# Kernel tuning notes

Hardware: AMD Instinct MI355X
Metric: run time of the kernel (lower is better)

Reference implementation:

```python
import jax, jax.numpy as jnp
import numpy as np
import math

D_FEAT = 256
D_EMB = 128
NUM_HEADS = 4
D_K = D_EMB // NUM_HEADS
N = 1024
SEQ = D_FEAT + 1


def _ln(x, g=None, b=None, eps=1e-5):
    m = jnp.mean(x, axis=-1, keepdims=True)
    v = jnp.mean((x - m) ** 2, axis=-1, keepdims=True)
    y = (x - m) / jnp.sqrt(v + eps)
    if g is None:
        return y
    return y * g + b


def setup_inputs() -> dict:
    key = jax.random.key(0)
    ks = jax.random.split(key, 16)
    s = 0.05  # init scale for linear weights
    inp = {
        "Z": jax.random.normal(ks[0], (N, D_FEAT), jnp.float32),
        "A_no_diag": jax.random.normal(ks[1], (SEQ, SEQ), jnp.float32),
        "feat_emb": jax.random.normal(ks[2], (D_FEAT, D_EMB), jnp.float32),
        "label_token": jax.random.normal(ks[3], (1, 1, D_EMB), jnp.float32),
        "Wq": jax.random.normal(ks[4], (D_EMB, D_EMB), jnp.float32) * s,
        "bq": jnp.zeros((D_EMB,), jnp.float32),
        "Wk": jax.random.normal(ks[5], (D_EMB, D_EMB), jnp.float32) * s,
        "bk": jnp.zeros((D_EMB,), jnp.float32),
        "Wv": jax.random.normal(ks[6], (D_EMB, D_EMB), jnp.float32) * s,
        "bv": jnp.zeros((D_EMB,), jnp.float32),
        "Wo": jax.random.normal(ks[7], (D_EMB, D_EMB), jnp.float32) * s,
        "bo": jnp.zeros((D_EMB,), jnp.float32),
        "W1": jax.random.normal(ks[8], (D_EMB, 2 * D_EMB), jnp.float32) * s,
        "b1": jnp.zeros((2 * D_EMB,), jnp.float32),
        "W2": jax.random.normal(ks[9], (2 * D_EMB, D_EMB), jnp.float32) * s,
        "b2": jnp.zeros((D_EMB,), jnp.float32),
        "g1": jnp.ones((D_EMB,), jnp.float32),
        "beta1": jnp.zeros((D_EMB,), jnp.float32),
        "g2": jnp.ones((D_EMB,), jnp.float32),
        "beta2": jnp.zeros((D_EMB,), jnp.float32),
        "alpha_res": jnp.asarray(0.5, jnp.float32),
    }
    return inp


def reference(Z, A_no_diag, feat_emb, label_token, Wq, bq, Wk, bk, Wv, bv,
              Wo, bo, W1, b1, W2, b2, g1, beta1, g2, beta2, alpha_res):
    n = Z.shape[0]
    # normalize raw features (no affine) over d_feat
    Z_norm = _ln(Z)                                   # [N, F]
    # outer-product feature embedding
    X_feats = Z_norm[:, :, None] * feat_emb[None]     # [N, F, E]
    label = jnp.broadcast_to(label_token, (n, 1, D_EMB))
    X = jnp.concatenate([X_feats, label], axis=1)     # [N, S, E]
    X_norm = _ln(X, g1, beta1)
    # QKV projections, split into heads
    Q = (X_norm @ Wq + bq).reshape(n, SEQ, NUM_HEADS, D_K)
    K = (X_norm @ Wk + bk).reshape(n, SEQ, NUM_HEADS, D_K)
    V = (X_norm @ Wv + bv).reshape(n, SEQ, NUM_HEADS, D_K)
    scores = jnp.einsum('nqhd,nkhd->nhqk', Q, K) / math.sqrt(D_K)
    # DAG additive log-mask
    cm = jnp.abs(A_no_diag).T
    c_max = jnp.max(cm)
    cm = jnp.where(c_max > 1e-6, cm / c_max, cm + 1e-3)
    di = jnp.arange(SEQ)
    cm = cm.at[di, di].set(1.0)
    dag_mask = jnp.log(cm + 1e-9)                     # [S, S]
    scores = scores + dag_mask[None, None]
    attn = jax.nn.softmax(scores, axis=-1)
    out = jnp.einsum('nhqk,nkhd->nqhd', attn, V).reshape(n, SEQ, D_EMB)
    out = out @ Wo + bo
    # FFN (dropout inactive in eval), exact GELU as torch default
    h = _ln(out, g2, beta2)
    ffn = jax.nn.gelu(h @ W1 + b1, approximate=False) @ W2 + b2
    Hn = out + ffn
    Z_final = alpha_res * Hn + X_norm
    return Z_final[:, -1, :]                          # [N, E]
```

## Files before the change

kernel.cpp:

```cpp
#include <hip/hip_runtime.h>
#include <hip/hip_bf16.h>
#include <math.h>

#define NSAMP 1024
#define F 256
#define E 128
#define SEQ 257
#define NH 4
#define DK 32

#define OFF_MASK   0
#define OFF_PMAX   264
#define OFF_A      512
#define OFF_B      1536
#define OFF_SCLAST 1540
#define OFF_CV     1544
#define OFF_VLAST  1672
#define OFF_XL     1800
#define OFF_VF     1928
#define OFF_MF     2184
#define OFF_UV     2560
#define OFF_SQ     35328
#define OFF_SK     35456
#define OFF_SCK    35584

__device__ inline float wave_sum(float v) {
#pragma unroll
    for (int off = 32; off >= 1; off >>= 1) v += __shfl_xor(v, off, 64);
    return v;
}
__device__ inline float wave_max(float v) {
#pragma unroll
    for (int off = 32; off >= 1; off >>= 1) v = fmaxf(v, __shfl_xor(v, off, 64));
    return v;
}
__device__ inline float gelu_exact(float x) {
    return 0.5f * x * (1.0f + erff(x * 0.7071067811865476f));
}

__global__ __launch_bounds__(128) void pre1_kernel(
    const float* __restrict__ A, const float* __restrict__ feat,
    const float* __restrict__ lab, const float* __restrict__ Wq,
    const float* __restrict__ bq, const float* __restrict__ Wk,
    const float* __restrict__ bk, const float* __restrict__ Wv,
    const float* __restrict__ bv, const float* __restrict__ g1,
    const float* __restrict__ beta1, float* __restrict__ ws)
{
    const int bid = blockIdx.x, tid = threadIdx.x;
    __shared__ float red[128];
    __shared__ float sv[128];

    if (bid < 128) {
        float m = 0.f;
        for (int i = bid * 128 + tid; i < SEQ * SEQ; i += 128 * 128)
            m = fmaxf(m, fabsf(A[i]));
        red[tid] = m;
        __syncthreads();
        for (int s = 64; s >= 1; s >>= 1) {
            if (tid < s) red[tid] = fmaxf(red[tid], red[tid + s]);
            __syncthreads();
        }
        if (tid == 0) ws[OFF_PMAX + bid] = red[0];
    } else if (bid < 384) {
        const int k = bid - 128;
        float f = feat[k * E + tid];
        red[tid] = f;
        __syncthreads();
        for (int s = 64; s >= 1; s >>= 1) { if (tid < s) red[tid] += red[tid + s]; __syncthreads(); }
        float mf = red[0] * (1.f / E);
        __syncthreads();
        float d = f - mf;
        red[tid] = d * d;
        __syncthreads();
        for (int s = 64; s >= 1; s >>= 1) { if (tid < s) red[tid] += red[tid + s]; __syncthreads(); }
        if (tid == 0) { ws[OFF_MF + k] = mf; ws[OFF_VF + k] = red[0] * (1.f / E); }
    } else {
        const int j = bid - 384;
        if (j < 3) {
            float lv = lab[tid];
            red[tid] = lv;
            __syncthreads();
            for (int s = 64; s >= 1; s >>= 1) { if (tid < s) red[tid] += red[tid + s]; __syncthreads(); }
            float lm = red[0] * (1.f / E);
            __syncthreads();
            float d = lv - lm;
            red[tid] = d * d;
            __syncthreads();
            for (int s = 64; s >= 1; s >>= 1) { if (tid < s) red[tid] += red[tid + s]; __syncthreads(); }
            float rstd = rsqrtf(red[0] * (1.f / E) + 1e-5f);
            __syncthreads();
            float x = d * rstd * g1[tid] + beta1[tid];
            sv[tid] = x;
            if (j == 0) ws[OFF_XL + tid] = x;
        } else {
            sv[tid] = beta1[tid];
        }
        __syncthreads();
        const float* W    = (j == 0) ? Wq : (j == 2 || j == 4) ? Wv : Wk;
        const float* bias = (j == 0) ? bq : (j == 2 || j == 4) ? bv : bk;
        float acc = 0.f;
#pragma unroll 8
        for (int e = 0; e < E; ++e) acc += sv[e] * W[e * E + tid];
        acc += bias[tid];
        const int off = (j == 0) ? OFF_SQ : (j == 1) ? OFF_SK : (j == 2) ? OFF_VLAST
                      : (j == 3) ? OFF_SCK : OFF_CV;
        ws[off + tid] = acc;
    }
}

__global__ __launch_bounds__(256) void pre23_kernel(
    const float* __restrict__ A, const float* __restrict__ feat,
    const float* __restrict__ g1, const float* __restrict__ Wk,
    const float* __restrict__ Wv, float* __restrict__ ws)
{
    const int bid = blockIdx.x, tid = threadIdx.x;
    __shared__ float su[128];
    __shared__ float sUK[128];
    __shared__ float red[256];

    if (bid < 256) {
        const int k = bid;
        if (tid < 128) {
            const float mf = ws[OFF_MF + k];
            su[tid] = (feat[k * E + tid] - mf) * g1[tid];
        }
        __syncthreads();
        {
            const int d = tid & 127;
            const float* W = (tid < 128) ? Wv : Wk;
            float acc = 0.f;
#pragma unroll 8
            for (int e = 0; e < E; ++e) acc += su[e] * W[e * E + d];
            if (tid < 128) ws[OFF_UV + k * E + d] = acc;
            else sUK[d] = acc;
        }
        __syncthreads();
        if (tid < 128) {
            float v = sUK[tid] * ws[OFF_SQ + tid];
#pragma unroll
            for (int off = 16; off >= 1; off >>= 1) v += __shfl_xor(v, off, 64);
            if ((tid & 31) == 0)
                ws[OFF_A + k * 4 + (tid >> 5)] = v * 0.17677669529663687f;
        }
    } else {
        float m = (tid < 128) ? ws[OFF_PMAX + tid] : 0.f;
        red[tid] = m;
        __syncthreads();
        for (int s = 128; s >= 1; s >>= 1) {
            if (tid < s) red[tid] = fmaxf(red[tid], red[tid + s]);
            __syncthreads();
        }
        const float cmax = red[0];
        {
            float v = fabsf(A[tid * SEQ + (SEQ - 1)]);
            float cmv = (cmax > 1e-6f) ? v / cmax : v + 1e-3f;
            ws[OFF_MASK + tid] = logf(cmv + 1e-9f);
        }
        if (tid < 128) su[tid]  = ws[OFF_SQ + tid];
        else           sUK[tid - 128] = ws[OFF_SK + tid - 128];
        if (tid < 128) red[tid] = ws[OFF_SCK + tid];
        __syncthreads();
        if (tid < NH) {
            const int h = tid;
            float bb = 0.f, sl = 0.f;
#pragma unroll
            for (int d = h * DK; d < (h + 1) * DK; ++d) {
                bb += su[d] * red[d];
                sl += su[d] * sUK[d];
            }
            const float rs = 0.17677669529663687f;
            ws[OFF_B + h] = bb * rs;
            ws[OFF_SCLAST + h] = sl * rs + logf(1.0f + 1e-9f);
        }
    }
}

__global__ __launch_bounds__(1024) void main_kernel(
    const float* __restrict__ Z, const float* __restrict__ Wo,
    const float* __restrict__ bo, const float* __restrict__ W1,
    const float* __restrict__ b1, const float* __restrict__ W2,
    const float* __restrict__ b2, const float* __restrict__ g2,
    const float* __restrict__ beta2, const float* __restrict__ alpha_p,
    const float* __restrict__ ws, float* __restrict__ out)
{
    const int tid = threadIdx.x;
    const int wv = tid >> 6, lane = tid & 63;
    const int n0 = blockIdx.x * 4;

    __shared__ float wm4[4][256][4];
    __shared__ float att4[128][4];
    __shared__ float oar[4][128];
    __shared__ float h24[128][4];
    __shared__ float gg4[256][4];
    __shared__ float red[4096];
    __shared__ float sSumP[4][4], sP256[4][4], sInv[4][4];

    if (wv < 4) {
        const int n = n0 + wv;
        float z[4];
#pragma unroll
        for (int i = 0; i < 4; ++i) z[i] = Z[n * F + lane + 64 * i];
        float sum = wave_sum(z[0] + z[1] + z[2] + z[3]);
        float mean = sum * (1.f / F);
        float ss = 0.f;
#pragma unroll
        for (int i = 0; i < 4; ++i) { float d = z[i] - mean; ss += d * d; }
        ss = wave_sum(ss);
        float rstd = rsqrtf(ss * (1.f / F) + 1e-5f);

        float tk[4], mk[4], areg[4][4];
#pragma unroll
        for (int i = 0; i < 4; ++i) {
            int k = lane + 64 * i;
            float s = (z[i] - mean) * rstd;
            float vf = ws[OFF_VF + k];
            tk[i] = s * rsqrtf(s * s * vf + 1e-5f);
            mk[i] = ws[OFF_MASK + k];
            float4 a4 = *(const float4*)(ws + OFF_A + k * 4);
            areg[i][0] = a4.x; areg[i][1] = a4.y; areg[i][2] = a4.z; areg[i][3] = a4.w;
        }
#pragma unroll
        for (int h = 0; h < 4; ++h) {
            float bh = ws[OFF_B + h];
            float scL = ws[OFF_SCLAST + h];
            float sc[4];
            float mx = -1e30f;
#pragma unroll
            for (int i = 0; i < 4; ++i) {
                sc[i] = tk[i] * areg[i][h] + bh + mk[i];
                mx = fmaxf(mx, sc[i]);
            }
            if (lane == 0) mx = fmaxf(mx, scL);
            mx = wave_max(mx);
            float local = 0.f;
            float p[4];
#pragma unroll
            for (int i = 0; i < 4; ++i) { p[i] = expf(sc[i] - mx); local += p[i]; }
            float sumP = wave_sum(local);
#pragma unroll
            for (int i = 0; i < 4; ++i) wm4[h][lane + 64 * i][wv] = p[i] * tk[i];
            if (lane == 0) {
                float p256 = expf(scL - mx);
                sSumP[wv][h] = sumP;
                sP256[wv][h] = p256;
                sInv[wv][h] = 1.f / (sumP + p256);
            }
        }
    }
    __syncthreads();

    const int g = tid >> 7;
    const int d = tid & 127;

    {
        const int h = d >> 5;
        float a0 = 0.f, a1 = 0.f, a2 = 0.f, a3 = 0.f;
        const float* uvp = ws + OFF_UV + (g * 32) * E + d;
#pragma unroll 8
        for (int kk = 0; kk < 32; ++kk) {
            float uv = uvp[kk * E];
            float4 w = *(const float4*)&wm4[h][g * 32 + kk][0];
            a0 += w.x * uv; a1 += w.y * uv; a2 += w.z * uv; a3 += w.w * uv;
        }
        float* r = red + g * 512 + d;
        r[0] = a0; r[128] = a1; r[256] = a2; r[384] = a3;
    }
    __syncthreads();
    if (tid < 512) {
        const int s = tid >> 7, dd = tid & 127, hh = dd >> 5;
        float v = 0.f;
#pragma unroll
        for (int gi = 0; gi < 8; ++gi) v += red[gi * 512 + s * 128 + dd];
        float cv = ws[OFF_CV + dd], vl = ws[OFF_VLAST + dd];
        att4[dd][s] = (v + sSumP[s][hh] * cv + sP256[s][hh] * vl) * sInv[s][hh];
    }
    __syncthreads();

    {
        float a0 = 0.f, a1 = 0.f, a2 = 0.f, a3 = 0.f;
        const float* wop = Wo + (g * 16) * E + d;
#pragma unroll 8
        for (int i = 0; i < 16; ++i) {
            float w = wop[i * E];
            float4 av = *(const float4*)&att4[g * 16 + i][0];
            a0 += av.x * w; a1 += av.y * w; a2 += av.z * w; a3 += av.w * w;
        }
        float* r = red + g * 512 + d;
        r[0] = a0; r[128] = a1; r[256] = a2; r[384] = a3;
    }
    __syncthreads();
    if (tid < 512) {
        const int s = tid >> 7, dd = tid & 127;
        float v = 0.f;
#pragma unroll
        for (int gi = 0; gi < 8; ++gi) v += red[gi * 512 + s * 128 + dd];
        oar[s][dd] = v + bo[dd];
    }
    __syncthreads();

    if (wv < 4) {
        float x0 = oar[wv][lane], x1 = oar[wv][lane + 64];
        float sum = wave_sum(x0 + x1);
        float mean = sum * (1.f / E);
        float d0 = x0 - mean, d1 = x1 - mean;
        float ss = wave_sum(d0 * d0 + d1 * d1);
        float rstd = rsqrtf(ss * (1.f / E) + 1e-5f);
        h24[lane][wv]      = d0 * rstd * g2[lane] + beta2[lane];
        h24[lane + 64][wv] = d1 * rstd * g2[lane + 64] + beta2[lane + 64];
    }
    __syncthreads();

    {
        const int grp = tid >> 8;
        const int j = tid & 255;
        float a0 = 0.f, a1 = 0.f, a2 = 0.f, a3 = 0.f;
        const float* w1p = W1 + (grp * 32) * (2 * E) + j;
#pragma unroll 8
        for (int i = 0; i < 32; ++i) {
            float w = w1p[i * (2 * E)];
            float4 hv = *(const float4*)&h24[grp * 32 + i][0];
            a0 += hv.x * w; a1 += hv.y * w; a2 += hv.z * w; a3 += hv.w * w;
        }
        float* r = red + grp * 1024 + j;
        r[0] = a0; r[256] = a1; r[512] = a2; r[768] = a3;
    }
    __syncthreads();
    {
        const int s = tid >> 8, j = tid & 255;
        float v = red[s * 256 + j] + red[1024 + s * 256 + j]
                + red[2048 + s * 256 + j] + red[3072 + s * 256 + j] + b1[j];
        gg4[j][s] = gelu_exact(v);
    }
    __syncthreads();

    {
        float a0 = 0.f, a1 = 0.f, a2 = 0.f, a3 = 0.f;
        const float* w2p = W2 + (g * 32) * E + d;
#pragma unroll 8
        for (int i = 0; i < 32; ++i) {
            float w = w2p[i * E];
            float4 gv = *(const float4*)&gg4[g * 32 + i][0];
            a0 += gv.x * w; a1 += gv.y * w; a2 += gv.z * w; a3 += gv.w * w;
        }
        float* r = red + g * 512 + d;
        r[0] = a0; r[128] = a1; r[256] = a2; r[384] = a3;
    }
    __syncthreads();
    if (tid < 512) {
        const int s = tid >> 7, dd = tid & 127;
        float f2 = b2[dd];
#pragma unroll
        for (int gi = 0; gi < 8; ++gi) f2 += red[gi * 512 + s * 128 + dd];
        float xl = ws[OFF_XL + dd];
        float alpha = alpha_p[0];
        out[(n0 + s) * E + dd] = alpha * (oar[s][dd] + f2) + xl;
    }
}

extern "C" void kernel_launch(void* const* d_in, const int* in_sizes, int n_in,
                              void* d_out, int out_size, void* d_ws, size_t ws_size,
                              hipStream_t stream) {
    const float* Z     = (const float*)d_in[0];
    const float* A     = (const float*)d_in[1];
    const float* feat  = (const float*)d_in[2];
    const float* lab   = (const float*)d_in[3];
    const float* Wq    = (const float*)d_in[4];
    const float* bq    = (const float*)d_in[5];
    const float* Wk    = (const float*)d_in[6];
    const float* bk    = (const float*)d_in[7];
    const float* Wv    = (const float*)d_in[8];
    const float* bv    = (const float*)d_in[9];
    const float* Wo    = (const float*)d_in[10];
    const float* bo    = (const float*)d_in[11];
    const float* W1    = (const float*)d_in[12];
    const float* b1    = (const float*)d_in[13];
    const float* W2    = (const float*)d_in[14];
    const float* b2    = (const float*)d_in[15];
    const float* g1    = (const float*)d_in[16];
    const float* beta1 = (const float*)d_in[17];
    const float* g2    = (const float*)d_in[18];
    const float* beta2 = (const float*)d_in[19];
    const float* alpha = (const float*)d_in[20];
    float* ws = (float*)d_ws;
    float* out = (float*)d_out;

    hipLaunchKernelGGL(pre1_kernel, dim3(389), dim3(128), 0, stream,
                       A, feat, lab, Wq, bq, Wk, bk, Wv, bv, g1, beta1, ws);
    hipLaunchKernelGGL(pre23_kernel, dim3(257), dim3(256), 0, stream,
                       A, feat, g1, Wk, Wv, ws);
    hipLaunchKernelGGL(main_kernel, dim3(NSAMP / 4), dim3(1024), 0, stream,
                       Z, Wo, bo, W1, b1, W2, b2, g2, beta2, alpha, ws, out);
}
```

Measured before the change: 25.77 us.

## Merge precompute kernels and fold mask/score setup into main kernel

Collapses the two precompute kernels into one by computing per-feature mean/var and the UV/UK projections in the same block. The DAG mask, the per-head bias terms and the per-feature attention scores move into the main kernel, where idle waves compute them into shared memory. The main kernel now processes 2 samples per block instead of 4, doubling the grid to 512 blocks. This removes a launch and a dependency stage, but each block redundantly recomputes the mask and scores, and the weights are reused across fewer samples per block.

```diff
diff --git a/kernel.cpp b/kernel.cpp
--- a/kernel.cpp
+++ b/kernel.cpp
@@ -9,20 +9,16 @@
 #define NH 4
 #define DK 32
 
-#define OFF_MASK   0
-#define OFF_PMAX   264
-#define OFF_A      512
-#define OFF_B      1536
-#define OFF_SCLAST 1540
-#define OFF_CV     1544
-#define OFF_VLAST  1672
-#define OFF_XL     1800
-#define OFF_VF     1928
-#define OFF_MF     2184
-#define OFF_UV     2560
-#define OFF_SQ     35328
-#define OFF_SK     35456
-#define OFF_SCK    35584
+#define OFF_PMAX   0
+#define OFF_VF     128
+#define OFF_XL     384
+#define OFF_CV     512
+#define OFF_VLAST  640
+#define OFF_SQ     768
+#define OFF_SK     896
+#define OFF_SCK    1024
+#define OFF_UV     1152
+#define OFF_UK     33920
 
 __device__ inline float wave_sum(float v) {
 #pragma unroll
@@ -38,7 +34,7 @@
     return 0.5f * x * (1.0f + erff(x * 0.7071067811865476f));
 }
 
-__global__ __launch_bounds__(128) void pre1_kernel(
+__global__ __launch_bounds__(256) void preA_kernel(
     const float* __restrict__ A, const float* __restrict__ feat,
     const float* __restrict__ lab, const float* __restrict__ Wq,
     const float* __restrict__ bq, const float* __restrict__ Wk,
@@ -47,155 +43,110 @@
     const float* __restrict__ beta1, float* __restrict__ ws)
 {
     const int bid = blockIdx.x, tid = threadIdx.x;
-    __shared__ float red[128];
+    __shared__ float red[256];
     __shared__ float sv[128];
 
-    if (bid < 128) {
+    if (bid < 256) {
+        const int k = bid;
+        float f = (tid < 128) ? feat[k * E + tid] : 0.f;
+        red[tid] = f;
+        __syncthreads();
+        for (int s = 128; s >= 1; s >>= 1) { if (tid < s) red[tid] += red[tid + s]; __syncthreads(); }
+        const float mf = red[0] * (1.f / E);
+        __syncthreads();
+        const float dd = f - mf;
+        red[tid] = (tid < 128) ? dd * dd : 0.f;
+        __syncthreads();
+        for (int s = 128; s >= 1; s >>= 1) { if (tid < s) red[tid] += red[tid + s]; __syncthreads(); }
+        if (tid == 0) ws[OFF_VF + k] = red[0] * (1.f / E);
+        if (tid < 128) sv[tid] = dd * g1[tid];
+        __syncthreads();
+        const int dcol = tid & 127;
+        const float* W = (tid < 128) ? Wv : Wk;
+        float acc = 0.f;
+#pragma unroll 8
+        for (int e = 0; e < E; ++e) acc += sv[e] * W[e * E + dcol];
+        if (tid < 128) ws[OFF_UV + k * E + dcol] = acc;
+        else           ws[OFF_UK + k * E + dcol] = acc;
+    } else if (bid < 384) {
         float m = 0.f;
-        for (int i = bid * 128 + tid; i < SEQ * SEQ; i += 128 * 128)
+        for (int i = (bid - 256) * 256 + tid; i < SEQ * SEQ; i += 128 * 256)
             m = fmaxf(m, fabsf(A[i]));
         red[tid] = m;
         __syncthreads();
-        for (int s = 64; s >= 1; s >>= 1) {
+        for (int s = 128; s >= 1; s >>= 1) {
             if (tid < s) red[tid] = fmaxf(red[tid], red[tid + s]);
             __syncthreads();
         }
-        if (tid == 0) ws[OFF_PMAX + bid] = red[0];
-    } else if (bid < 384) {
-        const int k = bid - 128;
-        float f = feat[k * E + tid];
-        red[tid] = f;
-        __syncthreads();
-        for (int s = 64; s >= 1; s >>= 1) { if (tid < s) red[tid] += red[tid + s]; __syncthreads(); }
-        float mf = red[0] * (1.f / E);
-        __syncthreads();
-        float d = f - mf;
-        red[tid] = d * d;
-        __syncthreads();
-        for (int s = 64; s >= 1; s >>= 1) { if (tid < s) red[tid] += red[tid + s]; __syncthreads(); }
-        if (tid == 0) { ws[OFF_MF + k] = mf; ws[OFF_VF + k] = red[0] * (1.f / E); }
+        if (tid == 0) ws[OFF_PMAX + (bid - 256)] = red[0];
     } else {
         const int j = bid - 384;
         if (j < 3) {
-            float lv = lab[tid];
+            float lv = (tid < 128) ? lab[tid] : 0.f;
             red[tid] = lv;
             __syncthreads();
-            for (int s = 64; s >= 1; s >>= 1) { if (tid < s) red[tid] += red[tid + s]; __syncthreads(); }
-            float lm = red[0] * (1.f / E);
-            __syncthreads();
-            float d = lv - lm;
-            red[tid] = d * d;
-            __syncthreads();
-            for (int s = 64; s >= 1; s >>= 1) { if (tid < s) red[tid] += red[tid + s]; __syncthreads(); }
-            float rstd = rsqrtf(red[0] * (1.f / E) + 1e-5f);
-            __syncthreads();
-            float x = d * rstd * g1[tid] + beta1[tid];
-            sv[tid] = x;
-            if (j == 0) ws[OFF_XL + tid] = x;
+            for (int s = 128; s >= 1; s >>= 1) { if (tid < s) red[tid] += red[tid + s]; __syncthreads(); }
+            const float lm = red[0] * (1.f / E);
+            __syncthreads();
+            const float dd = lv - lm;
+            red[tid] = (tid < 128) ? dd * dd : 0.f;
+            __syncthreads();
+            for (int s = 128; s >= 1; s >>= 1) { if (tid < s) red[tid] += red[tid + s]; __syncthreads(); }
+            const float rstd = rsqrtf(red[0] * (1.f / E) + 1e-5f);
+            __syncthreads();
+            if (tid < 128) {
+                float x = dd * rstd * g1[tid] + beta1[tid];
+                sv[tid] = x;
+                if (j == 0) ws[OFF_XL + tid] = x;
+            }
         } else {
-            sv[tid] = beta1[tid];
+            if (tid < 128) sv[tid] = beta1[tid];
         }
         __syncthreads();
         const float* W    = (j == 0) ? Wq : (j == 2 || j == 4) ? Wv : Wk;
         const float* bias = (j == 0) ? bq : (j == 2 || j == 4) ? bv : bk;
+        const int dcol = tid & 127;
+        const int e0 = (tid >> 7) * 64;
         float acc = 0.f;
 #pragma unroll 8
-        for (int e = 0; e < E; ++e) acc += sv[e] * W[e * E + tid];
-        acc += bias[tid];
-        const int off = (j == 0) ? OFF_SQ : (j == 1) ? OFF_SK : (j == 2) ? OFF_VLAST
-                      : (j == 3) ? OFF_SCK : OFF_CV;
-        ws[off + tid] = acc;
-    }
-}
-
-__global__ __launch_bounds__(256) void pre23_kernel(
-    const float* __restrict__ A, const float* __restrict__ feat,
-    const float* __restrict__ g1, const float* __restrict__ Wk,
-    const float* __restrict__ Wv, float* __restrict__ ws)
-{
-    const int bid = blockIdx.x, tid = threadIdx.x;
-    __shared__ float su[128];
-    __shared__ float sUK[128];
-    __shared__ float red[256];
-
-    if (bid < 256) {
-        const int k = bid;
+        for (int e = e0; e < e0 + 64; ++e) acc += sv[e] * W[e * E + dcol];
+        red[tid] = acc;
+        __syncthreads();
         if (tid < 128) {
-            const float mf = ws[OFF_MF + k];
-            su[tid] = (feat[k * E + tid] - mf) * g1[tid];
-        }
-        __syncthreads();
-        {
-            const int d = tid & 127;
-            const float* W = (tid < 128) ? Wv : Wk;
-            float acc = 0.f;
-#pragma unroll 8
-            for (int e = 0; e < E; ++e) acc += su[e] * W[e * E + d];
-            if (tid < 128) ws[OFF_UV + k * E + d] = acc;
-            else sUK[d] = acc;
-        }
-        __syncthreads();
-        if (tid < 128) {
-            float v = sUK[tid] * ws[OFF_SQ + tid];
-#pragma unroll
-            for (int off = 16; off >= 1; off >>= 1) v += __shfl_xor(v, off, 64);
-            if ((tid & 31) == 0)
-                ws[OFF_A + k * 4 + (tid >> 5)] = v * 0.17677669529663687f;
-        }
-    } else {
-        float m = (tid < 128) ? ws[OFF_PMAX + tid] : 0.f;
-        red[tid] = m;
-        __syncthreads();
-        for (int s = 128; s >= 1; s >>= 1) {
-            if (tid < s) red[tid] = fmaxf(red[tid], red[tid + s]);
-            __syncthreads();
-        }
-        const float cmax = red[0];
-        {
-            float v = fabsf(A[tid * SEQ + (SEQ - 1)]);
-            float cmv = (cmax > 1e-6f) ? v / cmax : v + 1e-3f;
-            ws[OFF_MASK + tid] = logf(cmv + 1e-9f);
-        }
-        if (tid < 128) su[tid]  = ws[OFF_SQ + tid];
-        else           sUK[tid - 128] = ws[OFF_SK + tid - 128];
-        if (tid < 128) red[tid] = ws[OFF_SCK + tid];
-        __syncthreads();
-        if (tid < NH) {
-            const int h = tid;
-            float bb = 0.f, sl = 0.f;
-#pragma unroll
-            for (int d = h * DK; d < (h + 1) * DK; ++d) {
-                bb += su[d] * red[d];
-                sl += su[d] * sUK[d];
-            }
-            const float rs = 0.17677669529663687f;
-            ws[OFF_B + h] = bb * rs;
-            ws[OFF_SCLAST + h] = sl * rs + logf(1.0f + 1e-9f);
-        }
-    }
-}
-
-__global__ __launch_bounds__(1024) void main_kernel(
-    const float* __restrict__ Z, const float* __restrict__ Wo,
-    const float* __restrict__ bo, const float* __restrict__ W1,
-    const float* __restrict__ b1, const float* __restrict__ W2,
-    const float* __restrict__ b2, const float* __restrict__ g2,
-    const float* __restrict__ beta2, const float* __restrict__ alpha_p,
-    const float* __restrict__ ws, float* __restrict__ out)
+            const int off = (j == 0) ? OFF_SQ : (j == 1) ? OFF_SK : (j == 2) ? OFF_VLAST
+                          : (j == 3) ? OFF_SCK : OFF_CV;
+            ws[off + tid] = red[tid] + red[tid + 128] + bias[tid];
+        }
+    }
+}
+
+__global__ __launch_bounds__(1024, 8) void main_kernel(
+    const float* __restrict__ Z, const float* __restrict__ A,
+    const float* __restrict__ Wo, const float* __restrict__ bo,
+    const float* __restrict__ W1, const float* __restrict__ b1,
+    const float* __restrict__ W2, const float* __restrict__ b2,
+    const float* __restrict__ g2, const float* __restrict__ beta2,
+    const float* __restrict__ alpha_p, const float* __restrict__ ws,
+    float* __restrict__ out)
 {
     const int tid = threadIdx.x;
     const int wv = tid >> 6, lane = tid & 63;
-    const int n0 = blockIdx.x * 4;
-
-    __shared__ float wm4[4][256][4];
-    __shared__ float att4[128][4];
-    __shared__ float oar[4][128];
-    __shared__ float h24[128][4];
-    __shared__ float gg4[256][4];
-    __shared__ float red[4096];
-    __shared__ float sSumP[4][4], sP256[4][4], sInv[4][4];
-
-    if (wv < 4) {
+    const int n0 = blockIdx.x * 2;
+
+    __shared__ __align__(16) float wm2[4][256][2];
+    __shared__ __align__(16) float sa[256][4];
+    __shared__ float smask[256];
+    __shared__ float sB[4], sScL[4];
+    __shared__ __align__(16) float red[2048];
+    __shared__ __align__(16) float att2[128][2];
+    __shared__ float oar[2][128];
+    __shared__ __align__(16) float h22[128][2];
+    __shared__ __align__(16) float gg2[256][2];
+    __shared__ float sSumP[2][4], sP256[2][4], sInv[2][4];
+
+    float tk[4];
+
+    if (wv < 2) {
         const int n = n0 + wv;
         float z[4];
 #pragma unroll
@@ -207,22 +158,74 @@
         for (int i = 0; i < 4; ++i) { float d = z[i] - mean; ss += d * d; }
         ss = wave_sum(ss);
         float rstd = rsqrtf(ss * (1.f / F) + 1e-5f);
-
-        float tk[4], mk[4], areg[4][4];
 #pragma unroll
         for (int i = 0; i < 4; ++i) {
             int k = lane + 64 * i;
             float s = (z[i] - mean) * rstd;
             float vf = ws[OFF_VF + k];
             tk[i] = s * rsqrtf(s * s * vf + 1e-5f);
-            mk[i] = ws[OFF_MASK + k];
-            float4 a4 = *(const float4*)(ws + OFF_A + k * 4);
+        }
+    } else if (wv == 2) {
+        float av[4];
+#pragma unroll
+        for (int q = 0; q < 4; ++q) av[q] = fabsf(A[(lane * 4 + q) * SEQ + (SEQ - 1)]);
+        float m = fmaxf(ws[OFF_PMAX + lane], ws[OFF_PMAX + lane + 64]);
+        m = wave_max(m);
+#pragma unroll
+        for (int q = 0; q < 4; ++q) {
+            float cmv = (m > 1e-6f) ? av[q] / m : av[q] + 1e-3f;
+            smask[lane * 4 + q] = logf(cmv + 1e-9f);
+        }
+    } else if (wv == 3) {
+        const int h = lane >> 4, i2 = lane & 15;
+        const int d0 = h * DK + 2 * i2, d1 = d0 + 1;
+        float q0 = ws[OFF_SQ + d0], q1 = ws[OFF_SQ + d1];
+        float pb = q0 * ws[OFF_SCK + d0] + q1 * ws[OFF_SCK + d1];
+        float ps = q0 * ws[OFF_SK + d0] + q1 * ws[OFF_SK + d1];
+#pragma unroll
+        for (int off = 8; off >= 1; off >>= 1) {
+            pb += __shfl_xor(pb, off, 64);
+            ps += __shfl_xor(ps, off, 64);
+        }
+        if (i2 == 0) {
+            const float rs = 0.17677669529663687f;
+            sB[h] = pb * rs;
+            sScL[h] = ps * rs + logf(1.0f + 1e-9f);
+        }
+    } else {
+        const int p0 = (wv - 4) * 64 + lane;
+#pragma unroll
+        for (int rep = 0; rep < 2; ++rep) {
+            const int q = p0 + rep * 768;
+            if (q < 1024) {
+                const int k = q >> 2, h = q & 3;
+                const float4* uk4 = (const float4*)(ws + OFF_UK + k * E + h * DK);
+                const float4* sq4 = (const float4*)(ws + OFF_SQ + h * DK);
+                float acc = 0.f;
+#pragma unroll
+                for (int i = 0; i < 8; ++i) {
+                    float4 u = uk4[i], s4 = sq4[i];
+                    acc += u.x * s4.x + u.y * s4.y + u.z * s4.z + u.w * s4.w;
+                }
+                sa[k][h] = acc * 0.17677669529663687f;
+            }
+        }
+    }
+    __syncthreads();
+
+    if (wv < 2) {
+        float mk[4], areg[4][4];
+#pragma unroll
+        for (int i = 0; i < 4; ++i) {
+            int k = lane + 64 * i;
+            mk[i] = smask[k];
+            float4 a4 = *(const float4*)&sa[k][0];
             areg[i][0] = a4.x; areg[i][1] = a4.y; areg[i][2] = a4.z; areg[i][3] = a4.w;
         }
 #pragma unroll
         for (int h = 0; h < 4; ++h) {
-            float bh = ws[OFF_B + h];
-            float scL = ws[OFF_SCLAST + h];
+            float bh = sB[h];
+            float scL = sScL[h];
             float sc[4];
             float mx = -1e30f;
 #pragma unroll
@@ -238,7 +241,7 @@
             for (int i = 0; i < 4; ++i) { p[i] = expf(sc[i] - mx); local += p[i]; }
             float sumP = wave_sum(local);
 #pragma unroll
-            for (int i = 0; i < 4; ++i) wm4[h][lane + 64 * i][wv] = p[i] * tk[i];
+            for (int i = 0; i < 4; ++i) wm2[h][lane + 64 * i][wv] = p[i] * tk[i];
             if (lane == 0) {
                 float p256 = expf(scL - mx);
                 sSumP[wv][h] = sumP;
@@ -254,103 +257,104 @@
 
     {
         const int h = d >> 5;
-        float a0 = 0.f, a1 = 0.f, a2 = 0.f, a3 = 0.f;
+        float a0 = 0.f, a1 = 0.f;
         const float* uvp = ws + OFF_UV + (g * 32) * E + d;
 #pragma unroll 8
         for (int kk = 0; kk < 32; ++kk) {
             float uv = uvp[kk * E];
-            float4 w = *(const float4*)&wm4[h][g * 32 + kk][0];
-            a0 += w.x * uv; a1 += w.y * uv; a2 += w.z * uv; a3 += w.w * uv;
-        }
-        float* r = red + g * 512 + d;
-        r[0] = a0; r[128] = a1; r[256] = a2; r[384] = a3;
-    }
-    __syncthreads();
-    if (tid < 512) {
+            float2 w = *(const float2*)&wm2[h][g * 32 + kk][0];
+            a0 += w.x * uv; a1 += w.y * uv;
+        }
+        float* r = red + g * 256 + d;
+        r[0] = a0; r[128] = a1;
+    }
+    __syncthreads();
+    if (tid < 256) {
         const int s = tid >> 7, dd = tid & 127, hh = dd >> 5;
         float v = 0.f;
 #pragma unroll
-        for (int gi = 0; gi < 8; ++gi) v += red[gi * 512 + s * 128 + dd];
+        for (int gi = 0; gi < 8; ++gi) v += red[gi * 256 + s * 128 + dd];
         float cv = ws[OFF_CV + dd], vl = ws[OFF_VLAST + dd];
-        att4[dd][s] = (v + sSumP[s][hh] * cv + sP256[s][hh] * vl) * sInv[s][hh];
+        att2[dd][s] = (v + sSumP[s][hh] * cv + sP256[s][hh] * vl) * sInv[s][hh];
     }
     __syncthreads();
 
     {
-        float a0 = 0.f, a1 = 0.f, a2 = 0.f, a3 = 0.f;
+        float a0 = 0.f, a1 = 0.f;
         const float* wop = Wo + (g * 16) * E + d;
 #pragma unroll 8
         for (int i = 0; i < 16; ++i) {
             float w = wop[i * E];
-            float4 av = *(const float4*)&att4[g * 16 + i][0];
-            a0 += av.x * w; a1 += av.y * w; a2 += av.z * w; a3 += av.w * w;
-        }
-        float* r = red + g * 512 + d;
-        r[0] = a0; r[128] = a1; r[256] = a2; r[384] = a3;
-    }
-    __syncthreads();
-    if (tid < 512) {
+            float2 av = *(const float2*)&att2[g * 16 + i][0];
+            a0 += av.x * w; a1 += av.y * w;
+        }
+        float* r = red + g * 256 + d;
+        r[0] = a0; r[128] = a1;
+    }
+    __syncthreads();
+    if (tid < 256) {
         const int s = tid >> 7, dd = tid & 127;
         float v = 0.f;
 #pragma unroll
-        for (int gi = 0; gi < 8; ++gi) v += red[gi * 512 + s * 128 + dd];
+        for (int gi = 0; gi < 8; ++gi) v += red[gi * 256 + s * 128 + dd];
         oar[s][dd] = v + bo[dd];
     }
     __syncthreads();
 
-    if (wv < 4) {
+    if (wv < 2) {
         float x0 = oar[wv][lane], x1 = oar[wv][lane + 64];
         float sum = wave_sum(x0 + x1);
         float mean = sum * (1.f / E);
         float d0 = x0 - mean, d1 = x1 - mean;
         float ss = wave_sum(d0 * d0 + d1 * d1);
         float rstd = rsqrtf(ss * (1.f / E) + 1e-5f);
-        h24[lane][wv]      = d0 * rstd * g2[lane] + beta2[lane];
-        h24[lane + 64][wv] = d1 * rstd * g2[lane + 64] + beta2[lane + 64];
+        h22[lane][wv]      = d0 * rstd * g2[lane] + beta2[lane];
+        h22[lane + 64][wv] = d1 * rstd * g2[lane + 64] + beta2[lane + 64];
     }
     __syncthreads();
 
     {
         const int grp = tid >> 8;
         const int j = tid & 255;
-        float a0 = 0.f, a1 = 0.f, a2 = 0.f, a3 = 0.f;
+        float a0 = 0.f, a1 = 0.f;
         const float* w1p = W1 + (grp * 32) * (2 * E) + j;
 #pragma unroll 8
         for (int i = 0; i < 32; ++i) {
             float w = w1p[i * (2 * E)];
-            float4 hv = *(const float4*)&h24[grp * 32 + i][0];
-            a0 += hv.x * w; a1 += hv.y * w; a2 += hv.z * w; a3 += hv.w * w;
-        }
-        float* r = red + grp * 1024 + j;
-        r[0] = a0; r[256] = a1; r[512] = a2; r[768] = a3;
-    }
-    __syncthreads();
+            float2 hv = *(const float2*)&h22[grp * 32 + i][0];
+            a0 += hv.x * w; a1 += hv.y * w;
+        }
+        float* r = red + grp * 512 + j;
+        r[0] = a0; r[256] = a1;
+    }
+    __syncthreads();
+    if (tid < 512) {
+        const int s = tid >> 8, j = tid & 255;
+        float v = b1[j];
+#pragma unroll
+        for (int gi = 0; gi < 4; ++gi) v += red[gi * 512 + s * 256 + j];
+        gg2[j][s] = gelu_exact(v);
+    }
+    __syncthreads();
+
     {
-        const int s = tid >> 8, j = tid & 255;
-        float v = red[s * 256 + j] + red[1024 + s * 256 + j]
-                + red[2048 + s * 256 + j] + red[3072 + s * 256 + j] + b1[j];
-        gg4[j][s] = gelu_exact(v);
-    }
-    __syncthreads();
-
-    {
-        float a0 = 0.f, a1 = 0.f, a2 = 0.f, a3 = 0.f;
+        float a0 = 0.f, a1 = 0.f;
         const float* w2p = W2 + (g * 32) * E + d;
 #pragma unroll 8
         for (int i = 0; i < 32; ++i) {
             float w = w2p[i * E];
-            float4 gv = *(const float4*)&gg4[g * 32 + i][0];
-            a0 += gv.x * w; a1 += gv.y * w; a2 += gv.z * w; a3 += gv.w * w;
-        }
-        float* r = red + g * 512 + d;
-        r[0] = a0; r[128] = a1; r[256] = a2; r[384] = a3;
-    }
-    __syncthreads();
-    if (tid < 512) {
+            float2 gv = *(const float2*)&gg2[g * 32 + i][0];
+            a0 += gv.x * w; a1 += gv.y * w;
+        }
+        float* r = red + g * 256 + d;
+        r[0] = a0; r[128] = a1;
+    }
+    __syncthreads();
+    if (tid < 256) {
         const int s = tid >> 7, dd = tid & 127;
         float f2 = b2[dd];
 #pragma unroll
-        for (int gi = 0; gi < 8; ++gi) f2 += red[gi * 512 + s * 128 + dd];
+        for (int gi = 0; gi < 8; ++gi) f2 += red[gi * 256 + s * 128 + dd];
         float xl = ws[OFF_XL + dd];
         float alpha = alpha_p[0];
         out[(n0 + s) * E + dd] = alpha * (oar[s][dd] + f2) + xl;
@@ -384,10 +388,8 @@
     float* ws = (float*)d_ws;
     float* out = (float*)d_out;
 
-    hipLaunchKernelGGL(pre1_kernel, dim3(389), dim3(128), 0, stream,
+    hipLaunchKernelGGL(preA_kernel, dim3(389), dim3(256), 0, stream,
                        A, feat, lab, Wq, bq, Wk, bk, Wv, bv, g1, beta1, ws);
-    hipLaunchKernelGGL(pre23_kernel, dim3(257), dim3(256), 0, stream,
-                       A, feat, g1, Wk, Wv, ws);
-    hipLaunchKernelGGL(main_kernel, dim3(NSAMP / 4), dim3(1024), 0, stream,
-                       Z, Wo, bo, W1, b1, W2, b2, g2, beta2, alpha, ws, out);
-}
+    hipLaunchKernelGGL(main_kernel, dim3(NSAMP / 2), dim3(1024), 0, stream,
+                       Z, A, Wo, bo, W1, b1, W2, b2, g2, beta2, alpha, ws, out);
+}
```

Result: slower. 37.03 us (+43.7%).
